# Optimization experiments

Hardware: AMD Instinct MI355X
Metric: run time of the kernel (lower is better)

The kernel has to match this reference:

```python
import jax, jax.numpy as jnp
import numpy as np

BN_EPS = 1e-5


def setup_inputs() -> dict:
    key = jax.random.key(0)
    ks = jax.random.split(key, 10)
    B, C, N = 16, 512, 4096
    Cr = C // 4
    s = 0.05
    return {
        "x": jax.random.normal(ks[0], (B, C, N), dtype=jnp.float32),
        # channel attention MLP (1x1 convs on pooled vector)
        "w1": jax.random.normal(ks[1], (Cr, C), dtype=jnp.float32) * s,
        "b1": jnp.zeros((Cr,), jnp.float32),
        "w2": jax.random.normal(ks[2], (C, Cr), dtype=jnp.float32) * s,
        "b2": jnp.zeros((C,), jnp.float32),
        # spatial attention branch
        "w3": jax.random.normal(ks[3], (Cr, C), dtype=jnp.float32) * s,
        "b3": jnp.zeros((Cr,), jnp.float32),
        "bn_gamma": jnp.ones((Cr,), jnp.float32),
        "bn_beta": jnp.zeros((Cr,), jnp.float32),
        "bn_mean": jnp.zeros((Cr,), jnp.float32),
        "bn_var": jnp.ones((Cr,), jnp.float32),
        "w4": jax.random.normal(ks[4], (1, Cr), dtype=jnp.float32) * s,
        "b4": jnp.zeros((1,), jnp.float32),
    }


def reference(x, w1, b1, w2, b2, w3, b3, bn_gamma, bn_beta, bn_mean, bn_var, w4, b4):
    # x: [B, C, N]; inference semantics (Dropout = identity, BN uses running stats)
    # ---- channel attention ----
    pooled = jnp.mean(x, axis=-1)                        # [B, C] (AdaptiveAvgPool1d(1))
    h = jax.nn.relu(pooled @ w1.T + b1)                  # [B, C/4]
    ca = jax.nn.sigmoid(h @ w2.T + b2)[:, :, None]       # [B, C, 1]
    x_ca = x * ca                                        # [B, C, N]
    # ---- spatial attention ----
    h2 = jnp.einsum('oc,bcn->bon', w3, x_ca) + b3[:, None]    # [B, C/4, N]
    inv = bn_gamma / jnp.sqrt(bn_var + BN_EPS)                 # [C/4]
    h2 = h2 * inv[:, None] + (bn_beta - bn_mean * inv)[:, None]
    h2 = jax.nn.relu(h2)
    sa = jax.nn.sigmoid(jnp.einsum('oc,bcn->bon', w4, h2) + b4[:, None])  # [B, 1, N]
    return x + x_ca * sa
```

## Files before the change

### kernel.cpp

```cpp
#include <hip/hip_runtime.h>
#include <math.h>

constexpr int B  = 16;
constexpr int C  = 512;
constexpr int N  = 4096;
constexpr int CR = 128;
constexpr int NT = 64;
constexpr int KC = 64;

typedef __attribute__((ext_vector_type(8))) short bf16x8;
typedef __attribute__((ext_vector_type(4))) float f32x4;

__device__ __forceinline__ float sigmoidf_(float v) {
    return 1.0f / (1.0f + __expf(-v));
}
__device__ __forceinline__ unsigned f2bf(float f) {
    unsigned u = __float_as_uint(f);
    u += 0x7fffu + ((u >> 16) & 1u);
    return u >> 16;
}

#define LGKM_BARRIER() do {                                   \
    asm volatile("s_waitcnt lgkmcnt(0)" ::: "memory");        \
    __builtin_amdgcn_s_barrier();                             \
    asm volatile("" ::: "memory");                            \
} while (0)

__global__ __launch_bounds__(256) void k_pre(
    const float* __restrict__ x, float* __restrict__ pooled,
    const float* __restrict__ w3, const float* __restrict__ b3,
    const float* __restrict__ gamma, const float* __restrict__ beta,
    const float* __restrict__ mean, const float* __restrict__ var,
    unsigned short* __restrict__ w3f, float* __restrict__ bias2)
{
    if (blockIdx.x < 2048) {
        int w    = threadIdx.x >> 6;
        int lane = threadIdx.x & 63;
        int row  = blockIdx.x * 4 + w;
        const float4* xr = (const float4*)(x + (size_t)row * N);
        float s = 0.f;
        #pragma unroll
        for (int i = 0; i < 16; ++i) {
            float4 v = xr[i * 64 + lane];
            s += v.x + v.y + v.z + v.w;
        }
        #pragma unroll
        for (int off = 32; off; off >>= 1) s += __shfl_xor(s, off, 64);
        if (lane == 0) pooled[row] = s * (1.0f / N);
    } else {
        int idx  = (blockIdx.x - 2048) * 256 + threadIdx.x;
        int g    = idx >> 6;
        int lane = idx & 63;
        int ck   = g >> 4;
        int kk   = (g >> 3) & 1;
        int ob   = g & 7;
        int o    = ob * 16 + (lane & 15);
        int c    = ck * 64 + kk * 32 + (lane >> 4) * 8;
        float inv = gamma[o] * rsqrtf(var[o] + 1e-5f);
        float4 a  = *(const float4*)(w3 + o * C + c);
        float4 bq = *(const float4*)(w3 + o * C + c + 4);
        unsigned r0 = f2bf(a.x * inv)  | (f2bf(a.y * inv) << 16);
        unsigned r1 = f2bf(a.z * inv)  | (f2bf(a.w * inv) << 16);
        unsigned r2 = f2bf(bq.x * inv) | (f2bf(bq.y * inv) << 16);
        unsigned r3 = f2bf(bq.z * inv) | (f2bf(bq.w * inv) << 16);
        *(uint4*)((char*)w3f + (size_t)idx * 16) = make_uint4(r0, r1, r2, r3);
        if (idx < CR) {
            float iv = gamma[idx] * rsqrtf(var[idx] + 1e-5f);
            bias2[idx] = b3[idx] * iv + beta[idx] - mean[idx] * iv;
        }
    }
}

__global__ __launch_bounds__(128) void k_ca(
    const float* __restrict__ pooled,
    const float* __restrict__ w1, const float* __restrict__ b1,
    const float* __restrict__ w2, const float* __restrict__ b2,
    float* __restrict__ ca)
{
    __shared__ float ps[C];
    __shared__ float hs[CR];
    int b = blockIdx.x, t = threadIdx.x;
    #pragma unroll
    for (int i = 0; i < 4; ++i) ps[t + i * 128] = pooled[b * C + t + i * 128];
    __syncthreads();

    float acc = b1[t];
    const float4* wr = (const float4*)(w1 + t * C);
    const float4* pr = (const float4*)ps;
    #pragma unroll 4
    for (int i = 0; i < C / 4; ++i) {
        float4 wv = wr[i], pv = pr[i];
        acc += wv.x * pv.x + wv.y * pv.y + wv.z * pv.z + wv.w * pv.w;
    }
    hs[t] = fmaxf(acc, 0.f);
    __syncthreads();

    #pragma unroll
    for (int k = 0; k < 4; ++k) {
        int c2 = t + k * 128;
        float a = b2[c2];
        const float4* w2r = (const float4*)(w2 + c2 * CR);
        const float4* hr  = (const float4*)hs;
        #pragma unroll 4
        for (int i = 0; i < CR / 4; ++i) {
            float4 wv = w2r[i], hv = hr[i];
            a += wv.x * hv.x + wv.y * hv.y + wv.z * hv.z + wv.w * hv.w;
        }
        ca[b * C + c2] = sigmoidf_(a);
    }
}

__global__ __launch_bounds__(256, 4) void k_main(
    const float* __restrict__ x, const float* __restrict__ ca,
    const unsigned short* __restrict__ w3f, const float* __restrict__ bias2,
    const float* __restrict__ w4, const float* __restrict__ b4,
    float* __restrict__ out)
{
    __shared__ __align__(16) short lds_x[2][NT * KC];
    __shared__ float ca_s[C];
    __shared__ __align__(16) float sa_s[NT];
    __shared__ float red[2][NT];
    __shared__ float bias2_s[CR];
    __shared__ float w4_s[CR];

    const int t    = threadIdx.x;
    const int lane = t & 63;
    const int w    = t >> 6;
    const int b    = blockIdx.y;
    const int n0   = blockIdx.x * NT;
    const int wo   = (w & 1) * 64;
    const int wn   = (w >> 1) * 32;
    const int ob0  = wo >> 4;

    const size_t xbase = (size_t)b * C * N + n0;
    const int ng = t & 31;
    const int cg = t >> 5;

    float2 xva[8], xvb[8];

#define LOADX(dst, CK) do { const int c0_ = (CK) * KC;                         \
    _Pragma("unroll") for (int ci = 0; ci < 8; ++ci)                           \
        dst[ci] = *(const float2*)(x + xbase + (size_t)(c0_ + cg * 8 + ci) * N + 2 * ng); \
} while (0)

#define CONVERT_WRITE(src, CK, BUF) do { const int c0_ = (CK) * KC;            \
    unsigned q0[4], q1[4];                                                     \
    _Pragma("unroll") for (int h = 0; h < 4; ++h) {                            \
        float s0 = ca_s[c0_ + cg * 8 + 2 * h];                                 \
        float s1 = ca_s[c0_ + cg * 8 + 2 * h + 1];                             \
        q0[h] = f2bf(src[2 * h].x * s0) | (f2bf(src[2 * h + 1].x * s1) << 16); \
        q1[h] = f2bf(src[2 * h].y * s0) | (f2bf(src[2 * h + 1].y * s1) << 16); \
    }                                                                          \
    int nl0 = 2 * ng, nl1 = 2 * ng + 1;                                        \
    int a0 = (nl0 * 128 + cg * 16) ^ ((nl0 & 7) << 4);                         \
    int a1 = (nl1 * 128 + cg * 16) ^ ((nl1 & 7) << 4);                         \
    *(uint4*)((char*)lds_x[BUF] + a0) = make_uint4(q0[0], q0[1], q0[2], q0[3]);\
    *(uint4*)((char*)lds_x[BUF] + a1) = make_uint4(q1[0], q1[1], q1[2], q1[3]);\
} while (0)

    LOADX(xva, 0);
    LOADX(xvb, 1);

    ca_s[t]       = ca[b * C + t];
    ca_s[t + 256] = ca[b * C + t + 256];
    if (t < CR) { bias2_s[t] = bias2[t]; w4_s[t] = w4[t]; }
    LGKM_BARRIER();

    CONVERT_WRITE(xva, 0, 0);

    f32x4 acc[4][2];
    #pragma unroll
    for (int i = 0; i < 4; ++i) { acc[i][0] = (f32x4)0.f; acc[i][1] = (f32x4)0.f; }

    const char* wf = (const char*)w3f;

    #pragma unroll
    for (int ck = 0; ck < 8; ++ck) {
        if (ck < 6) { if (ck & 1) LOADX(xvb, ck + 2); else LOADX(xva, ck + 2); }

        LGKM_BARRIER();

        #pragma unroll
        for (int kk = 0; kk < 2; ++kk) {
            bf16x8 af[4];
            #pragma unroll
            for (int i = 0; i < 4; ++i) {
                int g = ck * 16 + kk * 8 + ob0 + i;
                af[i] = *(const bf16x8*)(wf + (size_t)(g * 64 + lane) * 16);
            }
            bf16x8 bfr[2];
            #pragma unroll
            for (int j = 0; j < 2; ++j) {
                int br = wn + j * 16 + (lane & 15);
                int bb = (br * 128 + kk * 64 + (lane >> 4) * 16) ^ ((br & 7) << 4);
                bfr[j] = *(const bf16x8*)((const char*)lds_x[ck & 1] + bb);
            }
            #pragma unroll
            for (int i = 0; i < 4; ++i)
                #pragma unroll
                for (int j = 0; j < 2; ++j)
                    acc[i][j] = __builtin_amdgcn_mfma_f32_16x16x32_bf16(af[i], bfr[j], acc[i][j], 0, 0, 0);
        }
        if (ck < 7) { if (ck & 1) CONVERT_WRITE(xva, ck + 1, 0); else CONVERT_WRITE(xvb, ck + 1, 1); }
    }

    #pragma unroll
    for (int j = 0; j < 2; ++j) {
        float p = 0.f;
        #pragma unroll
        for (int i = 0; i < 4; ++i) {
            #pragma unroll
            for (int r = 0; r < 4; ++r) {
                int o = wo + i * 16 + (lane >> 4) * 4 + r;
                float hval = acc[i][j][r] + bias2_s[o];
                p = fmaf(w4_s[o], fmaxf(hval, 0.f), p);
            }
        }
        p += __shfl_xor(p, 16, 64);
        p += __shfl_xor(p, 32, 64);
        if (lane < 16) red[w & 1][wn + j * 16 + lane] = p;
    }
    __syncthreads();
    if (t < NT) sa_s[t] = sigmoidf_(red[0][t] + red[1][t] + b4[0]);
    __syncthreads();

    #pragma unroll 4
    for (int it = 0; it < 32; ++it) {
        int f4 = it * 256 + t;
        int c  = f4 >> 4;
        int n4 = f4 & 15;
        size_t off = xbase + (size_t)c * N + n4 * 4;
        float4 v = *(const float4*)(x + off);
        float cav = ca_s[c];
        float4 sv = *(const float4*)&sa_s[n4 * 4];
        float4 o4;
        o4.x = v.x * fmaf(cav, sv.x, 1.0f);
        o4.y = v.y * fmaf(cav, sv.y, 1.0f);
        o4.z = v.z * fmaf(cav, sv.z, 1.0f);
        o4.w = v.w * fmaf(cav, sv.w, 1.0f);
        *(float4*)(out + off) = o4;
    }
#undef LOADX
#undef CONVERT_WRITE
}

extern "C" void kernel_launch(void* const* d_in, const int* in_sizes, int n_in,
                              void* d_out, int out_size, void* d_ws, size_t ws_size,
                              hipStream_t stream)
{
    const float* x   = (const float*)d_in[0];
    const float* w1  = (const float*)d_in[1];
    const float* b1  = (const float*)d_in[2];
    const float* w2  = (const float*)d_in[3];
    const float* b2  = (const float*)d_in[4];
    const float* w3  = (const float*)d_in[5];
    const float* b3  = (const float*)d_in[6];
    const float* g   = (const float*)d_in[7];
    const float* be  = (const float*)d_in[8];
    const float* mn  = (const float*)d_in[9];
    const float* vr  = (const float*)d_in[10];
    const float* w4  = (const float*)d_in[11];
    const float* b4  = (const float*)d_in[12];
    float* out = (float*)d_out;

    float* ws     = (float*)d_ws;
    float* pooled = ws;
    float* ca     = ws + 8192;
    float* bias2  = ws + 16384;
    unsigned short* w3f = (unsigned short*)(ws + 16640);

    k_pre<<<2048 + 32, 256, 0, stream>>>(x, pooled, w3, b3, g, be, mn, vr, w3f, bias2);
    k_ca<<<B, 128, 0, stream>>>(pooled, w1, b1, w2, b2, ca);
    dim3 g3(N / NT, B);
    k_main<<<g3, 256, 0, stream>>>(x, ca, w3f, bias2, w4, b4, out);
}
```

Before: 125.0 us.

## Fold channel attention into per-batch scaled W3 and drop LDS staging in GEMM

A new kernel pre-scales the bf16 W3 fragments by the per-batch channel attention vector, giving one weight copy per batch. The main kernel then feeds raw x straight from global memory into MFMA B-fragments, converting to bf16 in registers with a three-stage register prefetch. This removes the LDS tile, the swizzled writes, the per-chunk barriers and the per-element ca multiply. The costs are an extra launch, a per-batch 128x512 bf16 weight buffer, strided scalar global loads of x, and each wave now computing all 128 output rows for its 16 columns.

After: 134.2 us. 7.3% more time.

```diff
diff --git a/kernel.cpp b/kernel.cpp
--- a/kernel.cpp
+++ b/kernel.cpp
@@ -6,10 +6,10 @@
 constexpr int N  = 4096;
 constexpr int CR = 128;
 constexpr int NT = 64;
-constexpr int KC = 64;
 
 typedef __attribute__((ext_vector_type(8))) short bf16x8;
 typedef __attribute__((ext_vector_type(4))) float f32x4;
+typedef __attribute__((ext_vector_type(4))) unsigned u32x4;
 
 __device__ __forceinline__ float sigmoidf_(float v) {
     return 1.0f / (1.0f + __expf(-v));
@@ -19,12 +19,6 @@
     u += 0x7fffu + ((u >> 16) & 1u);
     return u >> 16;
 }
-
-#define LGKM_BARRIER() do {                                   \
-    asm volatile("s_waitcnt lgkmcnt(0)" ::: "memory");        \
-    __builtin_amdgcn_s_barrier();                             \
-    asm volatile("" ::: "memory");                            \
-} while (0)
 
 __global__ __launch_bounds__(256) void k_pre(
     const float* __restrict__ x, float* __restrict__ pooled,
@@ -110,16 +104,50 @@
     }
 }
 
+__global__ __launch_bounds__(256) void k_wscale(
+    const unsigned short* __restrict__ w3f, const float* __restrict__ ca,
+    unsigned short* __restrict__ w3b)
+{
+    int idx  = blockIdx.x * 256 + threadIdx.x;
+    int b    = idx >> 13;
+    int i    = idx & 8191;
+    int g    = i >> 6;
+    int lane = i & 63;
+    int ck   = g >> 4;
+    int kk   = (g >> 3) & 1;
+    int c0   = ck * 64 + kk * 32 + ((lane >> 4) << 3);
+    uint4 wv = *(const uint4*)((const char*)w3f + (size_t)i * 16);
+    const float* cb = ca + b * C + c0;
+    float4 c01 = *(const float4*)cb;
+    float4 c23 = *(const float4*)(cb + 4);
+    uint4 ov;
+    {
+        float lo = __uint_as_float(wv.x << 16), hi = __uint_as_float(wv.x & 0xffff0000u);
+        ov.x = f2bf(lo * c01.x) | (f2bf(hi * c01.y) << 16);
+    }
+    {
+        float lo = __uint_as_float(wv.y << 16), hi = __uint_as_float(wv.y & 0xffff0000u);
+        ov.y = f2bf(lo * c01.z) | (f2bf(hi * c01.w) << 16);
+    }
+    {
+        float lo = __uint_as_float(wv.z << 16), hi = __uint_as_float(wv.z & 0xffff0000u);
+        ov.z = f2bf(lo * c23.x) | (f2bf(hi * c23.y) << 16);
+    }
+    {
+        float lo = __uint_as_float(wv.w << 16), hi = __uint_as_float(wv.w & 0xffff0000u);
+        ov.w = f2bf(lo * c23.z) | (f2bf(hi * c23.w) << 16);
+    }
+    *(uint4*)((char*)w3b + (size_t)idx * 16) = ov;
+}
+
 __global__ __launch_bounds__(256, 4) void k_main(
     const float* __restrict__ x, const float* __restrict__ ca,
-    const unsigned short* __restrict__ w3f, const float* __restrict__ bias2,
+    const unsigned short* __restrict__ w3b, const float* __restrict__ bias2,
     const float* __restrict__ w4, const float* __restrict__ b4,
     float* __restrict__ out)
 {
-    __shared__ __align__(16) short lds_x[2][NT * KC];
     __shared__ float ca_s[C];
     __shared__ __align__(16) float sa_s[NT];
-    __shared__ float red[2][NT];
     __shared__ float bias2_s[CR];
     __shared__ float w4_s[CR];
 
@@ -128,100 +156,63 @@
     const int w    = t >> 6;
     const int b    = blockIdx.y;
     const int n0   = blockIdx.x * NT;
-    const int wo   = (w & 1) * 64;
-    const int wn   = (w >> 1) * 32;
-    const int ob0  = wo >> 4;
-
-    const size_t xbase = (size_t)b * C * N + n0;
-    const int ng = t & 31;
-    const int cg = t >> 5;
-
-    float2 xva[8], xvb[8];
-
-#define LOADX(dst, CK) do { const int c0_ = (CK) * KC;                         \
-    _Pragma("unroll") for (int ci = 0; ci < 8; ++ci)                           \
-        dst[ci] = *(const float2*)(x + xbase + (size_t)(c0_ + cg * 8 + ci) * N + 2 * ng); \
-} while (0)
-
-#define CONVERT_WRITE(src, CK, BUF) do { const int c0_ = (CK) * KC;            \
-    unsigned q0[4], q1[4];                                                     \
-    _Pragma("unroll") for (int h = 0; h < 4; ++h) {                            \
-        float s0 = ca_s[c0_ + cg * 8 + 2 * h];                                 \
-        float s1 = ca_s[c0_ + cg * 8 + 2 * h + 1];                             \
-        q0[h] = f2bf(src[2 * h].x * s0) | (f2bf(src[2 * h + 1].x * s1) << 16); \
-        q1[h] = f2bf(src[2 * h].y * s0) | (f2bf(src[2 * h + 1].y * s1) << 16); \
-    }                                                                          \
-    int nl0 = 2 * ng, nl1 = 2 * ng + 1;                                        \
-    int a0 = (nl0 * 128 + cg * 16) ^ ((nl0 & 7) << 4);                         \
-    int a1 = (nl1 * 128 + cg * 16) ^ ((nl1 & 7) << 4);                         \
-    *(uint4*)((char*)lds_x[BUF] + a0) = make_uint4(q0[0], q0[1], q0[2], q0[3]);\
-    *(uint4*)((char*)lds_x[BUF] + a1) = make_uint4(q1[0], q1[1], q1[2], q1[3]);\
-} while (0)
-
-    LOADX(xva, 0);
-    LOADX(xvb, 1);
+    const int wn   = w * 16;
 
     ca_s[t]       = ca[b * C + t];
     ca_s[t + 256] = ca[b * C + t + 256];
     if (t < CR) { bias2_s[t] = bias2[t]; w4_s[t] = w4[t]; }
-    LGKM_BARRIER();
-
-    CONVERT_WRITE(xva, 0, 0);
-
-    f32x4 acc[4][2];
-    #pragma unroll
-    for (int i = 0; i < 4; ++i) { acc[i][0] = (f32x4)0.f; acc[i][1] = (f32x4)0.f; }
-
-    const char* wf = (const char*)w3f;
-
-    #pragma unroll
-    for (int ck = 0; ck < 8; ++ck) {
-        if (ck < 6) { if (ck & 1) LOADX(xvb, ck + 2); else LOADX(xva, ck + 2); }
-
-        LGKM_BARRIER();
-
-        #pragma unroll
-        for (int kk = 0; kk < 2; ++kk) {
-            bf16x8 af[4];
-            #pragma unroll
-            for (int i = 0; i < 4; ++i) {
-                int g = ck * 16 + kk * 8 + ob0 + i;
-                af[i] = *(const bf16x8*)(wf + (size_t)(g * 64 + lane) * 16);
-            }
-            bf16x8 bfr[2];
-            #pragma unroll
-            for (int j = 0; j < 2; ++j) {
-                int br = wn + j * 16 + (lane & 15);
-                int bb = (br * 128 + kk * 64 + (lane >> 4) * 16) ^ ((br & 7) << 4);
-                bfr[j] = *(const bf16x8*)((const char*)lds_x[ck & 1] + bb);
-            }
-            #pragma unroll
-            for (int i = 0; i < 4; ++i)
-                #pragma unroll
-                for (int j = 0; j < 2; ++j)
-                    acc[i][j] = __builtin_amdgcn_mfma_f32_16x16x32_bf16(af[i], bfr[j], acc[i][j], 0, 0, 0);
-        }
-        if (ck < 7) { if (ck & 1) CONVERT_WRITE(xva, ck + 1, 0); else CONVERT_WRITE(xvb, ck + 1, 1); }
-    }
-
-    #pragma unroll
-    for (int j = 0; j < 2; ++j) {
-        float p = 0.f;
-        #pragma unroll
-        for (int i = 0; i < 4; ++i) {
-            #pragma unroll
-            for (int r = 0; r < 4; ++r) {
-                int o = wo + i * 16 + (lane >> 4) * 4 + r;
-                float hval = acc[i][j][r] + bias2_s[o];
-                p = fmaf(w4_s[o], fmaxf(hval, 0.f), p);
-            }
-        }
-        p += __shfl_xor(p, 16, 64);
-        p += __shfl_xor(p, 32, 64);
-        if (lane < 16) red[w & 1][wn + j * 16 + lane] = p;
-    }
-    __syncthreads();
-    if (t < NT) sa_s[t] = sigmoidf_(red[0][t] + red[1][t] + b4[0]);
+
+    const size_t xbase = (size_t)b * C * N + n0;
+    const float* xcol = x + xbase + wn + (lane & 15) + (size_t)((lane >> 4) * 8) * N;
+    const char*  wb   = (const char*)w3b + (size_t)b * (CR * C * 2);
+    const int laneB   = lane * 16;
+
+    f32x4 acc[8];
+    #pragma unroll
+    for (int i = 0; i < 8; ++i) acc[i] = (f32x4)0.f;
+
+    float bst[3][8];
+
+#define BLOAD(K16, S) do {                                      \
+    _Pragma("unroll") for (int e = 0; e < 8; ++e)               \
+        bst[S][e] = xcol[(size_t)((K16) * 32 + e) * N];         \
+} while (0)
+
+    BLOAD(0, 0);
+    BLOAD(1, 1);
+
+    #pragma unroll
+    for (int k16 = 0; k16 < 16; ++k16) {
+        bf16x8 af[8];
+        #pragma unroll
+        for (int i = 0; i < 8; ++i)
+            af[i] = *(const bf16x8*)(wb + (size_t)((k16 * 8 + i) * 64) * 16 + laneB);
+        if (k16 < 14) BLOAD(k16 + 2, (k16 + 2) % 3);
+        const int s = k16 % 3;
+        union { u32x4 u; bf16x8 v; } bu;
+        #pragma unroll
+        for (int h = 0; h < 4; ++h)
+            bu.u[h] = f2bf(bst[s][2 * h]) | (f2bf(bst[s][2 * h + 1]) << 16);
+        #pragma unroll
+        for (int i = 0; i < 8; ++i)
+            acc[i] = __builtin_amdgcn_mfma_f32_16x16x32_bf16(af[i], bu.v, acc[i], 0, 0, 0);
+    }
+#undef BLOAD
+
+    __syncthreads();
+
+    float p = 0.f;
+    #pragma unroll
+    for (int i = 0; i < 8; ++i) {
+        #pragma unroll
+        for (int r = 0; r < 4; ++r) {
+            int o = i * 16 + ((lane >> 4) << 2) + r;
+            p = fmaf(w4_s[o], fmaxf(acc[i][r] + bias2_s[o], 0.f), p);
+        }
+    }
+    p += __shfl_xor(p, 16, 64);
+    p += __shfl_xor(p, 32, 64);
+    if (lane < 16) sa_s[wn + lane] = sigmoidf_(p + b4[0]);
     __syncthreads();
 
     #pragma unroll 4
@@ -240,8 +231,6 @@
         o4.w = v.w * fmaf(cav, sv.w, 1.0f);
         *(float4*)(out + off) = o4;
     }
-#undef LOADX
-#undef CONVERT_WRITE
 }
 
 extern "C" void kernel_launch(void* const* d_in, const int* in_sizes, int n_in,
@@ -268,9 +257,11 @@
     float* ca     = ws + 8192;
     float* bias2  = ws + 16384;
     unsigned short* w3f = (unsigned short*)(ws + 16640);
+    unsigned short* w3b = (unsigned short*)(ws + 16640 + 32768);
 
     k_pre<<<2048 + 32, 256, 0, stream>>>(x, pooled, w3, b3, g, be, mn, vr, w3f, bias2);
     k_ca<<<B, 128, 0, stream>>>(pooled, w1, b1, w2, b2, ca);
+    k_wscale<<<B * 8192 / 256, 256, 0, stream>>>(w3f, ca, w3b);
     dim3 g3(N / NT, B);
-    k_main<<<g3, 256, 0, stream>>>(x, ca, w3f, bias2, w4, b4, out);
-}
+    k_main<<<g3, 256, 0, stream>>>(x, ca, w3b, bias2, w4, b4, out);
+}
```
